# Kernel tuning notes

Hardware: AMD Instinct MI355X
Metric: run time of the kernel (lower is better)

Reference implementation:

```python
import jax, jax.numpy as jnp
import numpy as np

B, I, H, O, E, K = 1024, 512, 2048, 512, 8, 2


def setup_inputs() -> dict:
    key = jax.random.key(0)
    k = jax.random.split(key, 7)
    s = 0.02
    return {
        "x": jax.random.normal(k[0], (B, I), dtype=jnp.float32),
        "Wg": jax.random.normal(k[1], (I, E), dtype=jnp.float32) * s,
        "bg": jnp.zeros((E,), dtype=jnp.float32),
        "W1": jax.random.normal(k[2], (E, I, H), dtype=jnp.float32) * s,
        "b1": jnp.zeros((E, H), dtype=jnp.float32),
        "W2": jax.random.normal(k[3], (E, H, O), dtype=jnp.float32) * s,
        "b2": jnp.zeros((E, O), dtype=jnp.float32),
    }


def reference(x, Wg, bg, W1, b1, W2, b2):
    # Gating: linear -> softmax -> top-k -> renormalize (inference path,
    # no dynamic expert creation / sleep bookkeeping).
    logits = x @ Wg + bg                      # [B, E]
    probs = jax.nn.softmax(logits, axis=-1)
    top_w, top_i = jax.lax.top_k(probs, K)    # [B, K]
    top_w = top_w / jnp.sum(top_w, axis=-1, keepdims=True)
    # Dense combine weights: zero for unselected experts -> identical math to
    # the per-expert mask-gather / weighted scatter-add in the torch loop.
    combine = jnp.zeros((x.shape[0], W1.shape[0]), dtype=x.dtype)
    combine = combine.at[jnp.arange(x.shape[0])[:, None], top_i].add(top_w)  # [B, E]
    # Expert MLPs (Linear -> ReLU -> Linear), batched over experts.
    h = jax.nn.relu(jnp.einsum("bi,eih->beh", x, W1) + b1[None])  # [B, E, H]
    y = jnp.einsum("beh,eho->beo", h, W2) + b2[None]              # [B, E, O]
    out = jnp.einsum("be,beo->bo", combine, y)                    # [B, O]
    return out
```

## Files before the change

### kernel.cpp

```cpp
#include <hip/hip_runtime.h>
#include <math.h>


#define B_TOK 1024
#define I_DIM 512
#define H_DIM 2048
#define O_DIM 512
#define E_NUM 8
#define CAP   1024

#define WS_COUNTS   0
#define WS_TOK_E    64
#define WS_TOK_W    8256
#define WS_TOK_SLOT 16448
#define WS_XB       65536
#define WS_HB       (WS_XB + 1048576)
#define WS_Y2       (WS_HB + 33554432)

typedef __attribute__((ext_vector_type(8))) __bf16 bf16x8;
typedef __attribute__((ext_vector_type(4))) __bf16 bf16x4;
typedef __attribute__((ext_vector_type(2))) __bf16 bf16x2;
typedef __attribute__((ext_vector_type(4))) float f32x4;

#define MFMA16 __builtin_amdgcn_mfma_f32_16x16x32_bf16

__global__ __launch_bounds__(256) void gating_kernel(
    const float* __restrict__ x, const float* __restrict__ Wg,
    const float* __restrict__ bg, __bf16* __restrict__ xb,
    int* __restrict__ tok_e, float* __restrict__ tok_w)
{
    const int lane = threadIdx.x & 63;
    const int t = blockIdx.x * 4 + (threadIdx.x >> 6);
    const float4* x4 = (const float4*)(x + (size_t)t * I_DIM);
    float4 va = x4[lane], vb = x4[lane + 64];
    bf16x4 oa, ob;
    oa[0] = (__bf16)va.x; oa[1] = (__bf16)va.y;
    oa[2] = (__bf16)va.z; oa[3] = (__bf16)va.w;
    ob[0] = (__bf16)vb.x; ob[1] = (__bf16)vb.y;
    ob[2] = (__bf16)vb.z; ob[3] = (__bf16)vb.w;
    *(bf16x4*)(xb + (size_t)t * I_DIM + lane * 4) = oa;
    *(bf16x4*)(xb + (size_t)t * I_DIM + 256 + lane * 4) = ob;

    float acc[8];
#pragma unroll
    for (int e = 0; e < 8; ++e) acc[e] = 0.f;
    float xv[8] = {va.x, va.y, va.z, va.w, vb.x, vb.y, vb.z, vb.w};
#pragma unroll
    for (int u = 0; u < 8; ++u) {
        int i = (u < 4) ? (lane * 4 + u) : (256 + lane * 4 + u - 4);
        const float4* wr = (const float4*)(Wg + (size_t)i * 8);
        float4 wa = wr[0], wb2 = wr[1];
        acc[0] = fmaf(xv[u], wa.x, acc[0]);
        acc[1] = fmaf(xv[u], wa.y, acc[1]);
        acc[2] = fmaf(xv[u], wa.z, acc[2]);
        acc[3] = fmaf(xv[u], wa.w, acc[3]);
        acc[4] = fmaf(xv[u], wb2.x, acc[4]);
        acc[5] = fmaf(xv[u], wb2.y, acc[5]);
        acc[6] = fmaf(xv[u], wb2.z, acc[6]);
        acc[7] = fmaf(xv[u], wb2.w, acc[7]);
    }
#pragma unroll
    for (int off = 32; off > 0; off >>= 1)
#pragma unroll
        for (int e = 0; e < 8; ++e)
            acc[e] += __shfl_xor(acc[e], off, 64);
    if (lane == 0) {
        float l[8];
#pragma unroll
        for (int e = 0; e < 8; ++e) l[e] = acc[e] + bg[e];
        int e0 = 0;
        for (int e = 1; e < 8; ++e) if (l[e] > l[e0]) e0 = e;
        int e1 = (e0 == 0) ? 1 : 0;
        for (int e = 0; e < 8; ++e) {
            if (e == e0) continue;
            if (l[e] > l[e1]) e1 = e;
        }
        float w0 = 1.f / (1.f + expf(l[e1] - l[e0]));
        tok_e[t * 2]     = e0;
        tok_e[t * 2 + 1] = e1;
        tok_w[t * 2]     = w0;
        tok_w[t * 2 + 1] = 1.f - w0;
    }
}

template <bool IS_FC1>
__global__ __launch_bounds__(512) void moe_gemm(
    const __bf16* __restrict__ A, const float* __restrict__ Wf,
    const float* __restrict__ bias,
    int* __restrict__ counts, const int* __restrict__ tok_e,
    int* __restrict__ tok_slot,
    __bf16* __restrict__ hb, float* __restrict__ y2)
{
    constexpr int BN    = IS_FC1 ? 64 : 32;
    constexpr int KSPAN = IS_FC1 ? 512 : 1024;
    constexpr int BSTR  = KSPAN + 8;
    constexpr int NCH   = KSPAN / 256;
    constexpr int JN    = BN / 16;
    constexpr int C4N   = BN / 4;
    constexpr int NW    = IS_FC1 ? H_DIM : O_DIM;
    constexpr int ASTR  = IS_FC1 ? I_DIM : H_DIM;

    const int e  = blockIdx.z;
    const int kc = IS_FC1 ? 0 : (int)blockIdx.y;
    const int k0 = kc * KSPAN;
    const int n0 = blockIdx.x * BN;
    const int off = e * CAP;
    const float* W = Wf + (size_t)e * (IS_FC1 ? I_DIM * H_DIM : H_DIM * O_DIM);

    __shared__ __align__(16) __bf16 Bs[BN * BSTR];
    __shared__ int sl_tok[IS_FC1 ? CAP : 1];
    __shared__ int sMe;

    const int tid = threadIdx.x;
    const int lane = tid & 63, w = tid >> 6;
    const int l15 = lane & 15, q = lane >> 4;

    if (IS_FC1 && w == 0) {
        int cnt = 0;
#pragma unroll
        for (int b = 0; b < 2; ++b) {
            int vals[16];
#pragma unroll
            for (int c = 0; c < 16; ++c)
                vals[c] = tok_e[(b * 16 + c) * 64 + lane];
#pragma unroll
            for (int c = 0; c < 16; ++c) {
                const int gidx = (b * 16 + c) * 64 + lane;
                const bool hit = (vals[c] == e);
                const unsigned long long mk = __ballot(hit);
                if (hit) {
                    const int pos = cnt + __popcll(mk & ((1ull << lane) - 1));
                    sl_tok[pos] = gidx >> 1;
                    if (blockIdx.x == 0) tok_slot[gidx] = off + pos;
                }
                cnt += __popcll(mk);
            }
        }
        if (lane == 0) {
            sMe = cnt;
            if (blockIdx.x == 0) counts[e] = cnt;
        }
    }
    const int MeG = IS_FC1 ? 0 : counts[e];

    auto stage_chunk = [&](int ch) {
        const int kb = k0 + ch * 256;
#pragma unroll
        for (int i = 0; i < (128 * C4N) / 512; ++i) {
            const int u = tid + 512 * i;
            const int p = u / C4N, c4 = u % C4N;
            const float* wp = W + (size_t)(kb + 2 * p) * NW + n0 + c4 * 4;
            float4 r0 = *(const float4*)wp;
            float4 r1 = *(const float4*)(wp + NW);
            const float* f0 = (const float*)&r0;
            const float* f1 = (const float*)&r1;
#pragma unroll
            for (int j = 0; j < 4; ++j) {
                bf16x2 pk;
                pk[0] = (__bf16)f0[j];
                pk[1] = (__bf16)f1[j];
                *(bf16x2*)&Bs[(size_t)(c4 * 4 + j) * BSTR + ch * 256 + 2 * p] = pk;
            }
        }
    };

    stage_chunk(0);
    __syncthreads();
#pragma unroll
    for (int ch = 1; ch < NCH; ++ch) stage_chunk(ch);

    const int Me = IS_FC1 ? sMe : MeG;

    auto set_aptr = [&](int m0, const __bf16*& a0, const __bf16*& a1) {
        int mA = m0 + l15;      if (mA >= Me) mA = Me - 1;
        int mB = m0 + 16 + l15; if (mB >= Me) mB = Me - 1;
        if (IS_FC1) {
            a0 = A + (size_t)sl_tok[mA] * ASTR + q * 8;
            a1 = A + (size_t)sl_tok[mB] * ASTR + q * 8;
        } else {
            a0 = A + (size_t)(off + mA) * ASTR + k0 + q * 8;
            a1 = A + (size_t)(off + mB) * ASTR + k0 + q * 8;
        }
    };
    auto compute = [&](const __bf16* a0, const __bf16* a1,
                       f32x4 (&acc)[2][JN], int ks0, int ks1) {
#pragma unroll 4
        for (int ks = ks0; ks < ks1; ++ks) {
            bf16x8 af0 = *(const bf16x8*)(a0 + ks * 32);
            bf16x8 af1 = *(const bf16x8*)(a1 + ks * 32);
#pragma unroll
            for (int jj = 0; jj < JN; ++jj) {
                bf16x8 bf = *(const bf16x8*)
                    &Bs[(size_t)(jj * 16 + l15) * BSTR + ks * 32 + q * 8];
                acc[0][jj] = MFMA16(af0, bf, acc[0][jj], 0, 0, 0);
                acc[1][jj] = MFMA16(af1, bf, acc[1][jj], 0, 0, 0);
            }
        }
    };
    auto epilogue = [&](int m0, f32x4 (&acc)[2][JN]) {
#pragma unroll
        for (int jj = 0; jj < JN; ++jj) {
            const int gn = n0 + jj * 16 + l15;
            if (IS_FC1) {
                const float bv = bias[e * H_DIM + gn];
#pragma unroll
                for (int i = 0; i < 2; ++i)
#pragma unroll
                    for (int r = 0; r < 4; ++r) {
                        int m = m0 + i * 16 + q * 4 + r;
                        if (m < Me) {
                            float v = acc[i][jj][r] + bv;
                            hb[(size_t)(off + m) * H_DIM + gn] =
                                (__bf16)fmaxf(v, 0.f);
                        }
                    }
            } else {
#pragma unroll
                for (int i = 0; i < 2; ++i)
#pragma unroll
                    for (int r = 0; r < 4; ++r) {
                        int m = m0 + i * 16 + q * 4 + r;
                        if (m < Me)
                            y2[((size_t)kc * (E_NUM * CAP) + off + m) * O_DIM + gn] =
                                acc[i][jj][r];
                    }
            }
        }
    };

    const bool act0 = (w * 32 < Me);
    int m0 = w * 32;
    f32x4 acc[2][JN] = {};
    const __bf16 *a0 = nullptr, *a1 = nullptr;
    if (act0) {
        set_aptr(m0, a0, a1);
        compute(a0, a1, acc, 0, 8);
    }
    __syncthreads();
    if (act0) {
        compute(a0, a1, acc, 8, KSPAN / 32);
        epilogue(m0, acc);
    }
    for (m0 = w * 32 + 256; m0 < Me; m0 += 256) {
        f32x4 acc2[2][JN] = {};
        set_aptr(m0, a0, a1);
        compute(a0, a1, acc2, 0, KSPAN / 32);
        epilogue(m0, acc2);
    }
}

__global__ __launch_bounds__(256) void combine_kernel(
    const float* __restrict__ y2, const float* __restrict__ b2,
    const int* __restrict__ tok_slot, const int* __restrict__ tok_e,
    const float* __restrict__ tok_w, float* __restrict__ out)
{
    const int idx = blockIdx.x * 256 + threadIdx.x;
    const int t = idx >> 7;
    const int c = (idx & 127) * 4;
    float4 sum = {0.f, 0.f, 0.f, 0.f};
#pragma unroll
    for (int k = 0; k < 2; ++k) {
        const int s = tok_slot[t * 2 + k];
        const int e = tok_e[t * 2 + k];
        const float wgt = tok_w[t * 2 + k];
        float4 a = *(const float4*)(b2 + (size_t)e * O_DIM + c);
#pragma unroll
        for (int kc = 0; kc < 2; ++kc) {
            float4 v = *(const float4*)
                (y2 + ((size_t)kc * (E_NUM * CAP) + s) * O_DIM + c);
            a.x += v.x; a.y += v.y; a.z += v.z; a.w += v.w;
        }
        sum.x += wgt * a.x; sum.y += wgt * a.y;
        sum.z += wgt * a.z; sum.w += wgt * a.w;
    }
    *(float4*)(out + (size_t)t * O_DIM + c) = sum;
}

extern "C" void kernel_launch(void* const* d_in, const int* in_sizes, int n_in,
                              void* d_out, int out_size, void* d_ws, size_t ws_size,
                              hipStream_t stream)
{
    const float* x  = (const float*)d_in[0];
    const float* Wg = (const float*)d_in[1];
    const float* bg = (const float*)d_in[2];
    const float* W1 = (const float*)d_in[3];
    const float* b1 = (const float*)d_in[4];
    const float* W2 = (const float*)d_in[5];
    const float* b2 = (const float*)d_in[6];
    float* out = (float*)d_out;
    char* ws = (char*)d_ws;

    int*    counts   = (int*)(ws + WS_COUNTS);
    int*    tok_e    = (int*)(ws + WS_TOK_E);
    float*  tok_w    = (float*)(ws + WS_TOK_W);
    int*    tok_slot = (int*)(ws + WS_TOK_SLOT);
    __bf16* xb       = (__bf16*)(ws + WS_XB);
    __bf16* hb       = (__bf16*)(ws + WS_HB);
    float*  y2       = (float*)(ws + WS_Y2);

    gating_kernel<<<B_TOK / 4, 256, 0, stream>>>(x, Wg, bg, xb, tok_e, tok_w);
    moe_gemm<true><<<dim3(32, 1, 8), 512, 0, stream>>>(
        xb, W1, b1, counts, tok_e, tok_slot, hb, y2);
    moe_gemm<false><<<dim3(16, 2, 8), 512, 0, stream>>>(
        hb, W2, b2, counts, tok_e, tok_slot, hb, y2);
    combine_kernel<<<(B_TOK * O_DIM / 4) / 256, 256, 0, stream>>>(
        y2, b2, tok_slot, tok_e, tok_w, out);
}
```

Baseline: 155.7 us.

## Fuse MoE gating, FC1, FC2 and combine into one cooperative kernel

Replaces the four separate launches with a single cooperative kernel of 256 blocks that uses grid-wide syncs between the gating, FC1, FC2 and combine phases. During gating, half the warps pre-stage the first half of the W1 tile into shared memory so weight loading overlaps the routing work. The aim is to remove per-launch overhead and the idle gaps between kernels. In exchange it pays for three grid barriers and is limited to one block per CU. If the cooperative launch fails, the original multi-kernel path still runs.

```diff
diff --git a/kernel.cpp b/kernel.cpp
--- a/kernel.cpp
+++ b/kernel.cpp
@@ -1,5 +1,8 @@
 #include <hip/hip_runtime.h>
+#include <hip/hip_cooperative_groups.h>
 #include <math.h>
+
+namespace cg = cooperative_groups;
 
 
 #define B_TOK 1024
@@ -23,6 +26,339 @@
 typedef __attribute__((ext_vector_type(4))) float f32x4;
 
 #define MFMA16 __builtin_amdgcn_mfma_f32_16x16x32_bf16
+
+#define BSTR1 520
+#define BSTR2 1032
+#define SMEM_BS    (64 * BSTR1 * 2)
+#define SMEM_BYTES (SMEM_BS + CAP * 4 + 16)
+
+__global__ __launch_bounds__(512) void moe_fused(
+    const float* __restrict__ x, const float* __restrict__ Wg,
+    const float* __restrict__ bg, const float* __restrict__ W1f,
+    const float* __restrict__ b1, const float* __restrict__ W2f,
+    const float* __restrict__ b2, float* __restrict__ out,
+    char* __restrict__ ws)
+{
+    int*    counts   = (int*)(ws + WS_COUNTS);
+    int*    tok_e    = (int*)(ws + WS_TOK_E);
+    float*  tok_w    = (float*)(ws + WS_TOK_W);
+    int*    tok_slot = (int*)(ws + WS_TOK_SLOT);
+    __bf16* xb       = (__bf16*)(ws + WS_XB);
+    __bf16* hb       = (__bf16*)(ws + WS_HB);
+    float*  y2       = (float*)(ws + WS_Y2);
+
+    __shared__ __align__(16) char smem[SMEM_BYTES];
+    __bf16* Bs     = (__bf16*)smem;
+    int*    sl_tok = (int*)(smem + SMEM_BS);
+    int*    sMe    = (int*)(smem + SMEM_BS + CAP * 4);
+
+    cg::grid_group grid = cg::this_grid();
+    const int tid  = threadIdx.x;
+    const int lane = tid & 63;
+    const int w    = tid >> 6;
+    const int bid  = blockIdx.x;
+    const int l15  = lane & 15, q = lane >> 4;
+
+    const int e1  = bid >> 5, nx1 = bid & 31;
+    const int n01 = nx1 * 64;
+    const float* W1 = W1f + (size_t)e1 * (I_DIM * H_DIM);
+
+    if (w < 4) {
+        const int t = bid * 4 + w;
+        const float4* x4 = (const float4*)(x + (size_t)t * I_DIM);
+        float4 va = x4[lane], vb = x4[lane + 64];
+        bf16x4 oa, ob;
+        oa[0] = (__bf16)va.x; oa[1] = (__bf16)va.y;
+        oa[2] = (__bf16)va.z; oa[3] = (__bf16)va.w;
+        ob[0] = (__bf16)vb.x; ob[1] = (__bf16)vb.y;
+        ob[2] = (__bf16)vb.z; ob[3] = (__bf16)vb.w;
+        *(bf16x4*)(xb + (size_t)t * I_DIM + lane * 4) = oa;
+        *(bf16x4*)(xb + (size_t)t * I_DIM + 256 + lane * 4) = ob;
+
+        float gacc[8];
+#pragma unroll
+        for (int e = 0; e < 8; ++e) gacc[e] = 0.f;
+        float xv[8] = {va.x, va.y, va.z, va.w, vb.x, vb.y, vb.z, vb.w};
+#pragma unroll
+        for (int u = 0; u < 8; ++u) {
+            int i = (u < 4) ? (lane * 4 + u) : (256 + lane * 4 + u - 4);
+            const float4* wr = (const float4*)(Wg + (size_t)i * 8);
+            float4 wa = wr[0], wb2 = wr[1];
+            gacc[0] = fmaf(xv[u], wa.x, gacc[0]);
+            gacc[1] = fmaf(xv[u], wa.y, gacc[1]);
+            gacc[2] = fmaf(xv[u], wa.z, gacc[2]);
+            gacc[3] = fmaf(xv[u], wa.w, gacc[3]);
+            gacc[4] = fmaf(xv[u], wb2.x, gacc[4]);
+            gacc[5] = fmaf(xv[u], wb2.y, gacc[5]);
+            gacc[6] = fmaf(xv[u], wb2.z, gacc[6]);
+            gacc[7] = fmaf(xv[u], wb2.w, gacc[7]);
+        }
+#pragma unroll
+        for (int off = 32; off > 0; off >>= 1)
+#pragma unroll
+            for (int e = 0; e < 8; ++e)
+                gacc[e] += __shfl_xor(gacc[e], off, 64);
+        if (lane == 0) {
+            float l[8];
+#pragma unroll
+            for (int e = 0; e < 8; ++e) l[e] = gacc[e] + bg[e];
+            int E0 = 0;
+            for (int e = 1; e < 8; ++e) if (l[e] > l[E0]) E0 = e;
+            int E1 = (E0 == 0) ? 1 : 0;
+            for (int e = 0; e < 8; ++e) {
+                if (e == E0) continue;
+                if (l[e] > l[E1]) E1 = e;
+            }
+            float w0 = 1.f / (1.f + expf(l[E1] - l[E0]));
+            tok_e[t * 2]     = E0;
+            tok_e[t * 2 + 1] = E1;
+            tok_w[t * 2]     = w0;
+            tok_w[t * 2 + 1] = 1.f - w0;
+        }
+    } else {
+#pragma unroll
+        for (int i = 0; i < 8; ++i) {
+            const int u = (tid - 256) + 256 * i;
+            const int p = u >> 4, c4 = u & 15;
+            const float* wp = W1 + (size_t)(2 * p) * H_DIM + n01 + c4 * 4;
+            float4 r0 = *(const float4*)wp;
+            float4 r1 = *(const float4*)(wp + H_DIM);
+            const float* f0 = (const float*)&r0;
+            const float* f1 = (const float*)&r1;
+#pragma unroll
+            for (int j = 0; j < 4; ++j) {
+                bf16x2 pk;
+                pk[0] = (__bf16)f0[j];
+                pk[1] = (__bf16)f1[j];
+                *(bf16x2*)&Bs[(size_t)(c4 * 4 + j) * BSTR1 + 2 * p] = pk;
+            }
+        }
+    }
+    grid.sync();
+
+    {
+        if (w == 0) {
+            int cnt = 0;
+#pragma unroll
+            for (int b = 0; b < 2; ++b) {
+                int vals[16];
+#pragma unroll
+                for (int c = 0; c < 16; ++c)
+                    vals[c] = tok_e[(b * 16 + c) * 64 + lane];
+#pragma unroll
+                for (int c = 0; c < 16; ++c) {
+                    const int gidx = (b * 16 + c) * 64 + lane;
+                    const bool hit = (vals[c] == e1);
+                    const unsigned long long mk = __ballot(hit);
+                    if (hit) {
+                        const int pos = cnt + __popcll(mk & ((1ull << lane) - 1));
+                        sl_tok[pos] = gidx >> 1;
+                        if (nx1 == 0) tok_slot[gidx] = e1 * CAP + pos;
+                    }
+                    cnt += __popcll(mk);
+                }
+            }
+            if (lane == 0) {
+                sMe[0] = cnt;
+                if (nx1 == 0) counts[e1] = cnt;
+            }
+        }
+        __syncthreads();
+        const int Me  = sMe[0];
+        const int off = e1 * CAP;
+
+#pragma unroll
+        for (int i = 0; i < 4; ++i) {
+            const int u = tid + 512 * i;
+            const int p = u >> 4, c4 = u & 15;
+            const float* wp = W1 + (size_t)(256 + 2 * p) * H_DIM + n01 + c4 * 4;
+            float4 r0 = *(const float4*)wp;
+            float4 r1 = *(const float4*)(wp + H_DIM);
+            const float* f0 = (const float*)&r0;
+            const float* f1 = (const float*)&r1;
+#pragma unroll
+            for (int j = 0; j < 4; ++j) {
+                bf16x2 pk;
+                pk[0] = (__bf16)f0[j];
+                pk[1] = (__bf16)f1[j];
+                *(bf16x2*)&Bs[(size_t)(c4 * 4 + j) * BSTR1 + 256 + 2 * p] = pk;
+            }
+        }
+
+        auto aptrF = [&](int m0, const __bf16*& a0, const __bf16*& a1) {
+            int mA = m0 + l15;      if (mA >= Me) mA = Me - 1;
+            int mB = m0 + 16 + l15; if (mB >= Me) mB = Me - 1;
+            a0 = xb + (size_t)sl_tok[mA] * I_DIM + q * 8;
+            a1 = xb + (size_t)sl_tok[mB] * I_DIM + q * 8;
+        };
+        auto computeF = [&](const __bf16* a0, const __bf16* a1,
+                            f32x4 (&acc)[2][4], int ks0, int ks1) {
+#pragma unroll 4
+            for (int ks = ks0; ks < ks1; ++ks) {
+                bf16x8 af0 = *(const bf16x8*)(a0 + ks * 32);
+                bf16x8 af1 = *(const bf16x8*)(a1 + ks * 32);
+#pragma unroll
+                for (int jj = 0; jj < 4; ++jj) {
+                    bf16x8 bf = *(const bf16x8*)
+                        &Bs[(size_t)(jj * 16 + l15) * BSTR1 + ks * 32 + q * 8];
+                    acc[0][jj] = MFMA16(af0, bf, acc[0][jj], 0, 0, 0);
+                    acc[1][jj] = MFMA16(af1, bf, acc[1][jj], 0, 0, 0);
+                }
+            }
+        };
+        auto epiF = [&](int m0, f32x4 (&acc)[2][4]) {
+#pragma unroll
+            for (int jj = 0; jj < 4; ++jj) {
+                const int gn = n01 + jj * 16 + l15;
+                const float bv = b1[e1 * H_DIM + gn];
+#pragma unroll
+                for (int i2 = 0; i2 < 2; ++i2)
+#pragma unroll
+                    for (int r = 0; r < 4; ++r) {
+                        int m = m0 + i2 * 16 + q * 4 + r;
+                        if (m < Me) {
+                            float v = acc[i2][jj][r] + bv;
+                            hb[(size_t)(off + m) * H_DIM + gn] =
+                                (__bf16)fmaxf(v, 0.f);
+                        }
+                    }
+            }
+        };
+
+        const bool act0 = (w * 32 < Me);
+        f32x4 acc[2][4] = {};
+        const __bf16 *a0 = nullptr, *a1 = nullptr;
+        if (act0) {
+            aptrF(w * 32, a0, a1);
+            computeF(a0, a1, acc, 0, 8);
+        }
+        __syncthreads();
+        if (act0) {
+            computeF(a0, a1, acc, 8, 16);
+            epiF(w * 32, acc);
+        }
+        for (int m0 = w * 32 + 256; m0 < Me; m0 += 256) {
+            f32x4 acc2[2][4] = {};
+            aptrF(m0, a0, a1);
+            computeF(a0, a1, acc2, 0, 16);
+            epiF(m0, acc2);
+        }
+    }
+    grid.sync();
+
+    {
+        const int e  = bid >> 5, kc = (bid >> 4) & 1, nx = bid & 15;
+        const int Me = counts[e];
+        const int off = e * CAP;
+        const int k0 = kc * 1024;
+        const int n0 = nx * 32;
+        const float* W2 = W2f + (size_t)e * (H_DIM * O_DIM);
+
+        auto stage2 = [&](int ch) {
+            const int kb = k0 + ch * 256;
+#pragma unroll
+            for (int i = 0; i < 2; ++i) {
+                const int u = tid + 512 * i;
+                const int p = u >> 3, c4 = u & 7;
+                const float* wp = W2 + (size_t)(kb + 2 * p) * O_DIM + n0 + c4 * 4;
+                float4 r0 = *(const float4*)wp;
+                float4 r1 = *(const float4*)(wp + O_DIM);
+                const float* f0 = (const float*)&r0;
+                const float* f1 = (const float*)&r1;
+#pragma unroll
+                for (int j = 0; j < 4; ++j) {
+                    bf16x2 pk;
+                    pk[0] = (__bf16)f0[j];
+                    pk[1] = (__bf16)f1[j];
+                    *(bf16x2*)&Bs[(size_t)(c4 * 4 + j) * BSTR2 + ch * 256 + 2 * p] = pk;
+                }
+            }
+        };
+        stage2(0);
+        __syncthreads();
+        stage2(1); stage2(2); stage2(3);
+
+        auto aptr2 = [&](int m0, const __bf16*& a0, const __bf16*& a1) {
+            int mA = m0 + l15;      if (mA >= Me) mA = Me - 1;
+            int mB = m0 + 16 + l15; if (mB >= Me) mB = Me - 1;
+            a0 = hb + (size_t)(off + mA) * H_DIM + k0 + q * 8;
+            a1 = hb + (size_t)(off + mB) * H_DIM + k0 + q * 8;
+        };
+        auto compute2 = [&](const __bf16* a0, const __bf16* a1,
+                            f32x4 (&acc)[2][2], int ks0, int ks1) {
+#pragma unroll 4
+            for (int ks = ks0; ks < ks1; ++ks) {
+                bf16x8 af0 = *(const bf16x8*)(a0 + ks * 32);
+                bf16x8 af1 = *(const bf16x8*)(a1 + ks * 32);
+#pragma unroll
+                for (int jj = 0; jj < 2; ++jj) {
+                    bf16x8 bf = *(const bf16x8*)
+                        &Bs[(size_t)(jj * 16 + l15) * BSTR2 + ks * 32 + q * 8];
+                    acc[0][jj] = MFMA16(af0, bf, acc[0][jj], 0, 0, 0);
+                    acc[1][jj] = MFMA16(af1, bf, acc[1][jj], 0, 0, 0);
+                }
+            }
+        };
+        auto epi2 = [&](int m0, f32x4 (&acc)[2][2]) {
+#pragma unroll
+            for (int jj = 0; jj < 2; ++jj) {
+                const int gn = n0 + jj * 16 + l15;
+#pragma unroll
+                for (int i2 = 0; i2 < 2; ++i2)
+#pragma unroll
+                    for (int r = 0; r < 4; ++r) {
+                        int m = m0 + i2 * 16 + q * 4 + r;
+                        if (m < Me)
+                            y2[((size_t)kc * (E_NUM * CAP) + off + m) * O_DIM + gn] =
+                                acc[i2][jj][r];
+                    }
+            }
+        };
+
+        const bool act0 = (w * 32 < Me);
+        f32x4 acc[2][2] = {};
+        const __bf16 *a0 = nullptr, *a1 = nullptr;
+        if (act0) {
+            aptr2(w * 32, a0, a1);
+            compute2(a0, a1, acc, 0, 8);
+        }
+        __syncthreads();
+        if (act0) {
+            compute2(a0, a1, acc, 8, 32);
+            epi2(w * 32, acc);
+        }
+        for (int m0 = w * 32 + 256; m0 < Me; m0 += 256) {
+            f32x4 acc2[2][2] = {};
+            aptr2(m0, a0, a1);
+            compute2(a0, a1, acc2, 0, 32);
+            epi2(m0, acc2);
+        }
+    }
+    grid.sync();
+
+    {
+        const int idx = bid * 512 + tid;
+        const int t = idx >> 7;
+        const int c = (idx & 127) * 4;
+        float4 sum = {0.f, 0.f, 0.f, 0.f};
+#pragma unroll
+        for (int k = 0; k < 2; ++k) {
+            const int s = tok_slot[t * 2 + k];
+            const int e = tok_e[t * 2 + k];
+            const float wgt = tok_w[t * 2 + k];
+            float4 a = *(const float4*)(b2 + (size_t)e * O_DIM + c);
+#pragma unroll
+            for (int kc = 0; kc < 2; ++kc) {
+                float4 v = *(const float4*)
+                    (y2 + ((size_t)kc * (E_NUM * CAP) + s) * O_DIM + c);
+                a.x += v.x; a.y += v.y; a.z += v.z; a.w += v.w;
+            }
+            sum.x += wgt * a.x; sum.y += wgt * a.y;
+            sum.z += wgt * a.z; sum.w += wgt * a.w;
+        }
+        *(float4*)(out + (size_t)t * O_DIM + c) = sum;
+    }
+}
 
 __global__ __launch_bounds__(256) void gating_kernel(
     const float* __restrict__ x, const float* __restrict__ Wg,
@@ -40,7 +376,6 @@
     ob[2] = (__bf16)vb.z; ob[3] = (__bf16)vb.w;
     *(bf16x4*)(xb + (size_t)t * I_DIM + lane * 4) = oa;
     *(bf16x4*)(xb + (size_t)t * I_DIM + 256 + lane * 4) = ob;
-
     float acc[8];
 #pragma unroll
     for (int e = 0; e < 8; ++e) acc[e] = 0.f;
@@ -107,7 +442,7 @@
     const int off = e * CAP;
     const float* W = Wf + (size_t)e * (IS_FC1 ? I_DIM * H_DIM : H_DIM * O_DIM);
 
-    __shared__ __align__(16) __bf16 Bs[BN * BSTR];
+    __shared__ __align__(16) __bf16 Bsl[BN * BSTR];
     __shared__ int sl_tok[IS_FC1 ? CAP : 1];
     __shared__ int sMe;
 
@@ -159,7 +494,7 @@
                 bf16x2 pk;
                 pk[0] = (__bf16)f0[j];
                 pk[1] = (__bf16)f1[j];
-                *(bf16x2*)&Bs[(size_t)(c4 * 4 + j) * BSTR + ch * 256 + 2 * p] = pk;
+                *(bf16x2*)&Bsl[(size_t)(c4 * 4 + j) * BSTR + ch * 256 + 2 * p] = pk;
             }
         }
     };
@@ -191,7 +526,7 @@
 #pragma unroll
             for (int jj = 0; jj < JN; ++jj) {
                 bf16x8 bf = *(const bf16x8*)
-                    &Bs[(size_t)(jj * 16 + l15) * BSTR + ks * 32 + q * 8];
+                    &Bsl[(size_t)(jj * 16 + l15) * BSTR + ks * 32 + q * 8];
                 acc[0][jj] = MFMA16(af0, bf, acc[0][jj], 0, 0, 0);
                 acc[1][jj] = MFMA16(af1, bf, acc[1][jj], 0, 0, 0);
             }
@@ -290,6 +625,12 @@
     float* out = (float*)d_out;
     char* ws = (char*)d_ws;
 
+    void* args[] = {(void*)&x, (void*)&Wg, (void*)&bg, (void*)&W1, (void*)&b1,
+                    (void*)&W2, (void*)&b2, (void*)&out, (void*)&ws};
+    hipError_t err = hipLaunchCooperativeKernel(
+        (const void*)moe_fused, dim3(256), dim3(512), args, 0, stream);
+    if (err == hipSuccess) return;
+
     int*    counts   = (int*)(ws + WS_COUNTS);
     int*    tok_e    = (int*)(ws + WS_TOK_E);
     float*  tok_w    = (float*)(ws + WS_TOK_W);
```

Result: slower. 261.7 us (+68.1%).

## Pre-transpose expert weights to bf16 in a prep kernel and stream B from global

Applied to the files above, without the earlier changes.

Gating is merged into a new prep kernel that also converts W1 and W2 to bf16 and transposes them into workspace, using a padded shared-memory tile for the transpose. The FC1 and FC2 GEMMs no longer stage fp32 weights into LDS. They read the pre-transposed bf16 weights directly from global memory, and the grid is split over more M-blocks with 256-thread blocks. This moves the weight conversion out of the GEMMs and spreads work across more blocks, at the cost of an extra full pass writing weights to workspace and B-operand loads that now hit L2 instead of LDS.

```diff
diff --git a/kernel.cpp b/kernel.cpp
--- a/kernel.cpp
+++ b/kernel.cpp
@@ -14,8 +14,10 @@
 #define WS_TOK_W    8256
 #define WS_TOK_SLOT 16448
 #define WS_XB       65536
-#define WS_HB       (WS_XB + 1048576)
-#define WS_Y2       (WS_HB + 33554432)
+#define WS_W1T      1114112
+#define WS_W2T      17891328
+#define WS_HB       34668544
+#define WS_Y2       68222976
 
 typedef __attribute__((ext_vector_type(8))) __bf16 bf16x8;
 typedef __attribute__((ext_vector_type(4))) __bf16 bf16x4;
@@ -24,228 +26,246 @@
 
 #define MFMA16 __builtin_amdgcn_mfma_f32_16x16x32_bf16
 
-__global__ __launch_bounds__(256) void gating_kernel(
+__global__ __launch_bounds__(256) void prep_kernel(
     const float* __restrict__ x, const float* __restrict__ Wg,
-    const float* __restrict__ bg, __bf16* __restrict__ xb,
-    int* __restrict__ tok_e, float* __restrict__ tok_w)
-{
-    const int lane = threadIdx.x & 63;
-    const int t = blockIdx.x * 4 + (threadIdx.x >> 6);
-    const float4* x4 = (const float4*)(x + (size_t)t * I_DIM);
-    float4 va = x4[lane], vb = x4[lane + 64];
-    bf16x4 oa, ob;
-    oa[0] = (__bf16)va.x; oa[1] = (__bf16)va.y;
-    oa[2] = (__bf16)va.z; oa[3] = (__bf16)va.w;
-    ob[0] = (__bf16)vb.x; ob[1] = (__bf16)vb.y;
-    ob[2] = (__bf16)vb.z; ob[3] = (__bf16)vb.w;
-    *(bf16x4*)(xb + (size_t)t * I_DIM + lane * 4) = oa;
-    *(bf16x4*)(xb + (size_t)t * I_DIM + 256 + lane * 4) = ob;
-
-    float acc[8];
-#pragma unroll
-    for (int e = 0; e < 8; ++e) acc[e] = 0.f;
-    float xv[8] = {va.x, va.y, va.z, va.w, vb.x, vb.y, vb.z, vb.w};
-#pragma unroll
-    for (int u = 0; u < 8; ++u) {
-        int i = (u < 4) ? (lane * 4 + u) : (256 + lane * 4 + u - 4);
-        const float4* wr = (const float4*)(Wg + (size_t)i * 8);
-        float4 wa = wr[0], wb2 = wr[1];
-        acc[0] = fmaf(xv[u], wa.x, acc[0]);
-        acc[1] = fmaf(xv[u], wa.y, acc[1]);
-        acc[2] = fmaf(xv[u], wa.z, acc[2]);
-        acc[3] = fmaf(xv[u], wa.w, acc[3]);
-        acc[4] = fmaf(xv[u], wb2.x, acc[4]);
-        acc[5] = fmaf(xv[u], wb2.y, acc[5]);
-        acc[6] = fmaf(xv[u], wb2.z, acc[6]);
-        acc[7] = fmaf(xv[u], wb2.w, acc[7]);
-    }
-#pragma unroll
-    for (int off = 32; off > 0; off >>= 1)
-#pragma unroll
-        for (int e = 0; e < 8; ++e)
-            acc[e] += __shfl_xor(acc[e], off, 64);
-    if (lane == 0) {
-        float l[8];
-#pragma unroll
-        for (int e = 0; e < 8; ++e) l[e] = acc[e] + bg[e];
-        int e0 = 0;
-        for (int e = 1; e < 8; ++e) if (l[e] > l[e0]) e0 = e;
-        int e1 = (e0 == 0) ? 1 : 0;
-        for (int e = 0; e < 8; ++e) {
-            if (e == e0) continue;
-            if (l[e] > l[e1]) e1 = e;
-        }
-        float w0 = 1.f / (1.f + expf(l[e1] - l[e0]));
-        tok_e[t * 2]     = e0;
-        tok_e[t * 2 + 1] = e1;
-        tok_w[t * 2]     = w0;
-        tok_w[t * 2 + 1] = 1.f - w0;
-    }
-}
-
-template <bool IS_FC1>
-__global__ __launch_bounds__(512) void moe_gemm(
-    const __bf16* __restrict__ A, const float* __restrict__ Wf,
-    const float* __restrict__ bias,
-    int* __restrict__ counts, const int* __restrict__ tok_e,
-    int* __restrict__ tok_slot,
-    __bf16* __restrict__ hb, float* __restrict__ y2)
-{
-    constexpr int BN    = IS_FC1 ? 64 : 32;
-    constexpr int KSPAN = IS_FC1 ? 512 : 1024;
-    constexpr int BSTR  = KSPAN + 8;
-    constexpr int NCH   = KSPAN / 256;
-    constexpr int JN    = BN / 16;
-    constexpr int C4N   = BN / 4;
-    constexpr int NW    = IS_FC1 ? H_DIM : O_DIM;
-    constexpr int ASTR  = IS_FC1 ? I_DIM : H_DIM;
-
-    const int e  = blockIdx.z;
-    const int kc = IS_FC1 ? 0 : (int)blockIdx.y;
-    const int k0 = kc * KSPAN;
-    const int n0 = blockIdx.x * BN;
-    const int off = e * CAP;
-    const float* W = Wf + (size_t)e * (IS_FC1 ? I_DIM * H_DIM : H_DIM * O_DIM);
-
-    __shared__ __align__(16) __bf16 Bs[BN * BSTR];
-    __shared__ int sl_tok[IS_FC1 ? CAP : 1];
+    const float* __restrict__ bg, const float* __restrict__ W1f,
+    const float* __restrict__ W2f,
+    __bf16* __restrict__ xb, int* __restrict__ tok_e,
+    float* __restrict__ tok_w,
+    __bf16* __restrict__ W1T, __bf16* __restrict__ W2T)
+{
+    const int tid = threadIdx.x, lane = tid & 63, w = tid >> 6;
+    const int b = blockIdx.x;
+
+    if (b < 256) {
+        const int t = b * 4 + w;
+        const float4* x4 = (const float4*)(x + (size_t)t * I_DIM);
+        float4 va = x4[lane], vb = x4[lane + 64];
+        bf16x4 oa, ob;
+        oa[0] = (__bf16)va.x; oa[1] = (__bf16)va.y;
+        oa[2] = (__bf16)va.z; oa[3] = (__bf16)va.w;
+        ob[0] = (__bf16)vb.x; ob[1] = (__bf16)vb.y;
+        ob[2] = (__bf16)vb.z; ob[3] = (__bf16)vb.w;
+        *(bf16x4*)(xb + (size_t)t * I_DIM + lane * 4) = oa;
+        *(bf16x4*)(xb + (size_t)t * I_DIM + 256 + lane * 4) = ob;
+
+        float gacc[8];
+#pragma unroll
+        for (int e = 0; e < 8; ++e) gacc[e] = 0.f;
+        float xv[8] = {va.x, va.y, va.z, va.w, vb.x, vb.y, vb.z, vb.w};
+#pragma unroll
+        for (int u = 0; u < 8; ++u) {
+            int i = (u < 4) ? (lane * 4 + u) : (256 + lane * 4 + u - 4);
+            const float4* wr = (const float4*)(Wg + (size_t)i * 8);
+            float4 wa = wr[0], wb2 = wr[1];
+            gacc[0] = fmaf(xv[u], wa.x, gacc[0]);
+            gacc[1] = fmaf(xv[u], wa.y, gacc[1]);
+            gacc[2] = fmaf(xv[u], wa.z, gacc[2]);
+            gacc[3] = fmaf(xv[u], wa.w, gacc[3]);
+            gacc[4] = fmaf(xv[u], wb2.x, gacc[4]);
+            gacc[5] = fmaf(xv[u], wb2.y, gacc[5]);
+            gacc[6] = fmaf(xv[u], wb2.z, gacc[6]);
+            gacc[7] = fmaf(xv[u], wb2.w, gacc[7]);
+        }
+#pragma unroll
+        for (int off = 32; off > 0; off >>= 1)
+#pragma unroll
+            for (int e = 0; e < 8; ++e)
+                gacc[e] += __shfl_xor(gacc[e], off, 64);
+        if (lane == 0) {
+            float l[8];
+#pragma unroll
+            for (int e = 0; e < 8; ++e) l[e] = gacc[e] + bg[e];
+            int E0 = 0;
+            for (int e = 1; e < 8; ++e) if (l[e] > l[E0]) E0 = e;
+            int E1 = (E0 == 0) ? 1 : 0;
+            for (int e = 0; e < 8; ++e) {
+                if (e == E0) continue;
+                if (l[e] > l[E1]) E1 = e;
+            }
+            float w0 = 1.f / (1.f + expf(l[E1] - l[E0]));
+            tok_e[t * 2]     = E0;
+            tok_e[t * 2 + 1] = E1;
+            tok_w[t * 2]     = w0;
+            tok_w[t * 2 + 1] = 1.f - w0;
+        }
+    }
+
+    const float* src; __bf16* dst; int NWs, KT, k0, n0;
+    if (b < 512) {
+        const int e = b >> 6, t = b & 63;
+        src = W1f + (size_t)e * I_DIM * H_DIM;
+        dst = W1T + (size_t)e * H_DIM * I_DIM;
+        NWs = H_DIM; KT = I_DIM;
+        k0 = (t >> 3) * 64; n0 = (t & 7) * 256;
+    } else {
+        const int u = b - 512, e = u >> 6, t = u & 63;
+        src = W2f + (size_t)e * H_DIM * O_DIM;
+        dst = W2T + (size_t)e * O_DIM * H_DIM;
+        NWs = O_DIM; KT = H_DIM;
+        k0 = (t >> 1) * 64; n0 = (t & 1) * 256;
+    }
+    __shared__ uint32_t T[256 * 33];
+#pragma unroll
+    for (int i = 0; i < 8; ++i) {
+        const int u = tid + 256 * i;
+        const int p = u >> 6, c4 = u & 63;
+        const float* wp = src + (size_t)(k0 + 2 * p) * NWs + n0 + c4 * 4;
+        float4 r0 = *(const float4*)wp;
+        float4 r1 = *(const float4*)(wp + NWs);
+        const float* f0 = (const float*)&r0;
+        const float* f1 = (const float*)&r1;
+#pragma unroll
+        for (int j = 0; j < 4; ++j) {
+            bf16x2 pk;
+            pk[0] = (__bf16)f0[j];
+            pk[1] = (__bf16)f1[j];
+            *(bf16x2*)&T[(c4 * 4 + j) * 33 + p] = pk;
+        }
+    }
+    __syncthreads();
+#pragma unroll
+    for (int i = 0; i < 8; ++i) {
+        const int v = tid + 256 * i;
+        const int n = v >> 3, s = v & 7;
+        uint4 d;
+        d.x = T[n * 33 + s * 4 + 0];
+        d.y = T[n * 33 + s * 4 + 1];
+        d.z = T[n * 33 + s * 4 + 2];
+        d.w = T[n * 33 + s * 4 + 3];
+        *(uint4*)(dst + (size_t)(n0 + n) * KT + k0 + s * 8) = d;
+    }
+}
+
+__global__ __launch_bounds__(256) void fc1_kernel(
+    const __bf16* __restrict__ xb, const __bf16* __restrict__ W1T,
+    const float* __restrict__ b1, const int* __restrict__ tok_e,
+    int* __restrict__ counts, int* __restrict__ tok_slot,
+    __bf16* __restrict__ hb)
+{
+    const int tid = threadIdx.x, lane = tid & 63, w = tid >> 6;
+    const int l15 = lane & 15, q = lane >> 4;
+    const int e = blockIdx.z, my = blockIdx.y, nx = blockIdx.x;
+    const int n0 = nx * 64;
+
+    __shared__ int sl[CAP];
     __shared__ int sMe;
 
-    const int tid = threadIdx.x;
-    const int lane = tid & 63, w = tid >> 6;
-    const int l15 = lane & 15, q = lane >> 4;
-
-    if (IS_FC1 && w == 0) {
+    if (w == 0) {
         int cnt = 0;
 #pragma unroll
-        for (int b = 0; b < 2; ++b) {
+        for (int bb = 0; bb < 2; ++bb) {
             int vals[16];
 #pragma unroll
             for (int c = 0; c < 16; ++c)
-                vals[c] = tok_e[(b * 16 + c) * 64 + lane];
+                vals[c] = tok_e[(bb * 16 + c) * 64 + lane];
 #pragma unroll
             for (int c = 0; c < 16; ++c) {
-                const int gidx = (b * 16 + c) * 64 + lane;
+                const int gidx = (bb * 16 + c) * 64 + lane;
                 const bool hit = (vals[c] == e);
                 const unsigned long long mk = __ballot(hit);
                 if (hit) {
                     const int pos = cnt + __popcll(mk & ((1ull << lane) - 1));
-                    sl_tok[pos] = gidx >> 1;
-                    if (blockIdx.x == 0) tok_slot[gidx] = off + pos;
+                    sl[pos] = gidx >> 1;
+                    if (nx == 0 && my == 0) tok_slot[gidx] = e * CAP + pos;
                 }
                 cnt += __popcll(mk);
             }
         }
         if (lane == 0) {
             sMe = cnt;
-            if (blockIdx.x == 0) counts[e] = cnt;
-        }
-    }
-    const int MeG = IS_FC1 ? 0 : counts[e];
-
-    auto stage_chunk = [&](int ch) {
-        const int kb = k0 + ch * 256;
-#pragma unroll
-        for (int i = 0; i < (128 * C4N) / 512; ++i) {
-            const int u = tid + 512 * i;
-            const int p = u / C4N, c4 = u % C4N;
-            const float* wp = W + (size_t)(kb + 2 * p) * NW + n0 + c4 * 4;
-            float4 r0 = *(const float4*)wp;
-            float4 r1 = *(const float4*)(wp + NW);
-            const float* f0 = (const float*)&r0;
-            const float* f1 = (const float*)&r1;
-#pragma unroll
-            for (int j = 0; j < 4; ++j) {
-                bf16x2 pk;
-                pk[0] = (__bf16)f0[j];
-                pk[1] = (__bf16)f1[j];
-                *(bf16x2*)&Bs[(size_t)(c4 * 4 + j) * BSTR + ch * 256 + 2 * p] = pk;
-            }
-        }
-    };
-
-    stage_chunk(0);
+            if (nx == 0 && my == 0) counts[e] = cnt;
+        }
+    }
     __syncthreads();
-#pragma unroll
-    for (int ch = 1; ch < NCH; ++ch) stage_chunk(ch);
-
-    const int Me = IS_FC1 ? sMe : MeG;
-
-    auto set_aptr = [&](int m0, const __bf16*& a0, const __bf16*& a1) {
+    const int Me = sMe;
+
+    const __bf16* Wt  = W1T + (size_t)e * H_DIM * I_DIM;
+    const __bf16* bp0 = Wt + (size_t)(n0 + l15) * I_DIM + q * 8;
+
+    for (int m0 = my * 128 + w * 32; m0 < Me; m0 += 256) {
         int mA = m0 + l15;      if (mA >= Me) mA = Me - 1;
         int mB = m0 + 16 + l15; if (mB >= Me) mB = Me - 1;
-        if (IS_FC1) {
-            a0 = A + (size_t)sl_tok[mA] * ASTR + q * 8;
-            a1 = A + (size_t)sl_tok[mB] * ASTR + q * 8;
-        } else {
-            a0 = A + (size_t)(off + mA) * ASTR + k0 + q * 8;
-            a1 = A + (size_t)(off + mB) * ASTR + k0 + q * 8;
-        }
-    };
-    auto compute = [&](const __bf16* a0, const __bf16* a1,
-                       f32x4 (&acc)[2][JN], int ks0, int ks1) {
+        const __bf16* a0 = xb + (size_t)sl[mA] * I_DIM + q * 8;
+        const __bf16* a1 = xb + (size_t)sl[mB] * I_DIM + q * 8;
+        f32x4 acc[2][4] = {};
 #pragma unroll 4
-        for (int ks = ks0; ks < ks1; ++ks) {
+        for (int ks = 0; ks < 16; ++ks) {
             bf16x8 af0 = *(const bf16x8*)(a0 + ks * 32);
             bf16x8 af1 = *(const bf16x8*)(a1 + ks * 32);
 #pragma unroll
-            for (int jj = 0; jj < JN; ++jj) {
-                bf16x8 bf = *(const bf16x8*)
-                    &Bs[(size_t)(jj * 16 + l15) * BSTR + ks * 32 + q * 8];
+            for (int jj = 0; jj < 4; ++jj) {
+                bf16x8 bf = *(const bf16x8*)(bp0 + (size_t)jj * 16 * I_DIM + ks * 32);
                 acc[0][jj] = MFMA16(af0, bf, acc[0][jj], 0, 0, 0);
                 acc[1][jj] = MFMA16(af1, bf, acc[1][jj], 0, 0, 0);
             }
         }
-    };
-    auto epilogue = [&](int m0, f32x4 (&acc)[2][JN]) {
-#pragma unroll
-        for (int jj = 0; jj < JN; ++jj) {
+#pragma unroll
+        for (int jj = 0; jj < 4; ++jj) {
             const int gn = n0 + jj * 16 + l15;
-            if (IS_FC1) {
-                const float bv = bias[e * H_DIM + gn];
-#pragma unroll
-                for (int i = 0; i < 2; ++i)
-#pragma unroll
-                    for (int r = 0; r < 4; ++r) {
-                        int m = m0 + i * 16 + q * 4 + r;
-                        if (m < Me) {
-                            float v = acc[i][jj][r] + bv;
-                            hb[(size_t)(off + m) * H_DIM + gn] =
-                                (__bf16)fmaxf(v, 0.f);
-                        }
+            const float bv = b1[e * H_DIM + gn];
+#pragma unroll
+            for (int i = 0; i < 2; ++i)
+#pragma unroll
+                for (int r = 0; r < 4; ++r) {
+                    int m = m0 + i * 16 + q * 4 + r;
+                    if (m < Me) {
+                        float v = acc[i][jj][r] + bv;
+                        hb[(size_t)(e * CAP + m) * H_DIM + gn] =
+                            (__bf16)fmaxf(v, 0.f);
                     }
-            } else {
-#pragma unroll
-                for (int i = 0; i < 2; ++i)
-#pragma unroll
-                    for (int r = 0; r < 4; ++r) {
-                        int m = m0 + i * 16 + q * 4 + r;
-                        if (m < Me)
-                            y2[((size_t)kc * (E_NUM * CAP) + off + m) * O_DIM + gn] =
-                                acc[i][jj][r];
-                    }
+                }
+        }
+    }
+}
+
+__global__ __launch_bounds__(256) void fc2_kernel(
+    const __bf16* __restrict__ hb, const __bf16* __restrict__ W2T,
+    const int* __restrict__ counts, float* __restrict__ y2)
+{
+    const int tid = threadIdx.x, lane = tid & 63, w = tid >> 6;
+    const int l15 = lane & 15, q = lane >> 4;
+    const int e = blockIdx.z;
+    const int my = blockIdx.y & 1, kc = blockIdx.y >> 1;
+    const int n0 = blockIdx.x * 32;
+    const int k0 = kc * 1024;
+
+    const int Me = counts[e];
+    if (Me == 0) return;
+
+    const __bf16* Wt  = W2T + (size_t)e * O_DIM * H_DIM;
+    const __bf16* bp0 = Wt + (size_t)(n0 + l15) * H_DIM + k0 + q * 8;
+
+    for (int m0 = my * 128 + w * 32; m0 < Me; m0 += 256) {
+        int mA = m0 + l15;      if (mA >= Me) mA = Me - 1;
+        int mB = m0 + 16 + l15; if (mB >= Me) mB = Me - 1;
+        const __bf16* a0 = hb + (size_t)(e * CAP + mA) * H_DIM + k0 + q * 8;
+        const __bf16* a1 = hb + (size_t)(e * CAP + mB) * H_DIM + k0 + q * 8;
+        f32x4 acc[2][2] = {};
+#pragma unroll 4
+        for (int ks = 0; ks < 32; ++ks) {
+            bf16x8 af0 = *(const bf16x8*)(a0 + ks * 32);
+            bf16x8 af1 = *(const bf16x8*)(a1 + ks * 32);
+#pragma unroll
+            for (int jj = 0; jj < 2; ++jj) {
+                bf16x8 bf = *(const bf16x8*)(bp0 + (size_t)jj * 16 * H_DIM + ks * 32);
+                acc[0][jj] = MFMA16(af0, bf, acc[0][jj], 0, 0, 0);
+                acc[1][jj] = MFMA16(af1, bf, acc[1][jj], 0, 0, 0);
             }
         }
-    };
-
-    const bool act0 = (w * 32 < Me);
-    int m0 = w * 32;
-    f32x4 acc[2][JN] = {};
-    const __bf16 *a0 = nullptr, *a1 = nullptr;
-    if (act0) {
-        set_aptr(m0, a0, a1);
-        compute(a0, a1, acc, 0, 8);
-    }
-    __syncthreads();
-    if (act0) {
-        compute(a0, a1, acc, 8, KSPAN / 32);
-        epilogue(m0, acc);
-    }
-    for (m0 = w * 32 + 256; m0 < Me; m0 += 256) {
-        f32x4 acc2[2][JN] = {};
-        set_aptr(m0, a0, a1);
-        compute(a0, a1, acc2, 0, KSPAN / 32);
-        epilogue(m0, acc2);
+#pragma unroll
+        for (int jj = 0; jj < 2; ++jj) {
+            const int gn = n0 + jj * 16 + l15;
+#pragma unroll
+            for (int i = 0; i < 2; ++i)
+#pragma unroll
+                for (int r = 0; r < 4; ++r) {
+                    int m = m0 + i * 16 + q * 4 + r;
+                    if (m < Me)
+                        y2[((size_t)kc * (E_NUM * CAP) + e * CAP + m) * O_DIM + gn] =
+                            acc[i][jj][r];
+                }
+        }
     }
 }
 
@@ -295,14 +315,16 @@
     float*  tok_w    = (float*)(ws + WS_TOK_W);
     int*    tok_slot = (int*)(ws + WS_TOK_SLOT);
     __bf16* xb       = (__bf16*)(ws + WS_XB);
+    __bf16* W1T      = (__bf16*)(ws + WS_W1T);
+    __bf16* W2T      = (__bf16*)(ws + WS_W2T);
     __bf16* hb       = (__bf16*)(ws + WS_HB);
     float*  y2       = (float*)(ws + WS_Y2);
 
-    gating_kernel<<<B_TOK / 4, 256, 0, stream>>>(x, Wg, bg, xb, tok_e, tok_w);
-    moe_gemm<true><<<dim3(32, 1, 8), 512, 0, stream>>>(
-        xb, W1, b1, counts, tok_e, tok_slot, hb, y2);
-    moe_gemm<false><<<dim3(16, 2, 8), 512, 0, stream>>>(
-        hb, W2, b2, counts, tok_e, tok_slot, hb, y2);
+    prep_kernel<<<1024, 256, 0, stream>>>(x, Wg, bg, W1, W2,
+                                          xb, tok_e, tok_w, W1T, W2T);
+    fc1_kernel<<<dim3(32, 2, 8), 256, 0, stream>>>(
+        xb, W1T, b1, tok_e, counts, tok_slot, hb);
+    fc2_kernel<<<dim3(16, 4, 8), 256, 0, stream>>>(hb, W2T, counts, y2);
     combine_kernel<<<(B_TOK * O_DIM / 4) / 256, 256, 0, stream>>>(
         y2, b2, tok_slot, tok_e, tok_w, out);
 }
```

Result: slower. 195.9 us (+25.9%).

## Shrink MoE GEMM tiles to 32 columns, split FC2 K four ways, flatten grid

Applied to the files above, without the earlier changes.

Both expert GEMMs now use a uniform 32-column by 512-K tile, so FC1 launches 512 blocks instead of 256 and FC2 splits K into four chunks (512 blocks instead of 256). The grid is flattened with the expert index in the low bits, and the overlapped weight-staging/compute phase is removed in favour of one staging pass then compute. Launch bounds request higher occupancy. The intent is to fill more CUs and cut per-block weight staging. In exchange, FC1 redoes the token scan and A-row gathers in twice as many blocks, and the combine kernel reads four fp32 partial buffers instead of two.

```diff
diff --git a/kernel.cpp b/kernel.cpp
--- a/kernel.cpp
+++ b/kernel.cpp
@@ -14,8 +14,8 @@
 #define WS_TOK_W    8256
 #define WS_TOK_SLOT 16448
 #define WS_XB       65536
-#define WS_HB       (WS_XB + 1048576)
-#define WS_Y2       (WS_HB + 33554432)
+#define WS_HB       1114112
+#define WS_Y4       34668544
 
 typedef __attribute__((ext_vector_type(8))) __bf16 bf16x8;
 typedef __attribute__((ext_vector_type(4))) __bf16 bf16x4;
@@ -23,6 +23,7 @@
 typedef __attribute__((ext_vector_type(4))) float f32x4;
 
 #define MFMA16 __builtin_amdgcn_mfma_f32_16x16x32_bf16
+#define BSTR 520
 
 __global__ __launch_bounds__(256) void gating_kernel(
     const float* __restrict__ x, const float* __restrict__ Wg,
@@ -84,132 +85,118 @@
 }
 
 template <bool IS_FC1>
-__global__ __launch_bounds__(512) void moe_gemm(
+__global__ __launch_bounds__(512, 4) void moe_gemm(
     const __bf16* __restrict__ A, const float* __restrict__ Wf,
     const float* __restrict__ bias,
     int* __restrict__ counts, const int* __restrict__ tok_e,
     int* __restrict__ tok_slot,
-    __bf16* __restrict__ hb, float* __restrict__ y2)
-{
-    constexpr int BN    = IS_FC1 ? 64 : 32;
-    constexpr int KSPAN = IS_FC1 ? 512 : 1024;
-    constexpr int BSTR  = KSPAN + 8;
-    constexpr int NCH   = KSPAN / 256;
-    constexpr int JN    = BN / 16;
-    constexpr int C4N   = BN / 4;
-    constexpr int NW    = IS_FC1 ? H_DIM : O_DIM;
-    constexpr int ASTR  = IS_FC1 ? I_DIM : H_DIM;
-
-    const int e  = blockIdx.z;
-    const int kc = IS_FC1 ? 0 : (int)blockIdx.y;
-    const int k0 = kc * KSPAN;
-    const int n0 = blockIdx.x * BN;
+    __bf16* __restrict__ hb, float* __restrict__ y4)
+{
+    constexpr int NW   = IS_FC1 ? H_DIM : O_DIM;
+    constexpr int ASTR = IS_FC1 ? I_DIM : H_DIM;
+
+    const int bid = blockIdx.x;
+    const int e = bid & 7;
+    const int r = bid >> 3;
+    const int nx = IS_FC1 ? r : (r & 15);
+    const int kc = IS_FC1 ? 0 : (r >> 4);
+    const int n0 = nx * 32;
+    const int kb = kc * 512;
     const int off = e * CAP;
     const float* W = Wf + (size_t)e * (IS_FC1 ? I_DIM * H_DIM : H_DIM * O_DIM);
 
-    __shared__ __align__(16) __bf16 Bs[BN * BSTR];
-    __shared__ int sl_tok[IS_FC1 ? CAP : 1];
+    __shared__ __align__(16) __bf16 Bs[32 * BSTR];
+    __shared__ int sl[IS_FC1 ? CAP : 1];
     __shared__ int sMe;
 
     const int tid = threadIdx.x;
     const int lane = tid & 63, w = tid >> 6;
     const int l15 = lane & 15, q = lane >> 4;
 
+#pragma unroll
+    for (int i = 0; i < 4; ++i) {
+        const int u = tid + 512 * i;
+        const int p = u >> 3, c4 = u & 7;
+        const float* wp = W + (size_t)(kb + 2 * p) * NW + n0 + c4 * 4;
+        float4 r0 = *(const float4*)wp;
+        float4 r1 = *(const float4*)(wp + NW);
+        const float* f0 = (const float*)&r0;
+        const float* f1 = (const float*)&r1;
+#pragma unroll
+        for (int j = 0; j < 4; ++j) {
+            bf16x2 pk;
+            pk[0] = (__bf16)f0[j];
+            pk[1] = (__bf16)f1[j];
+            *(bf16x2*)&Bs[(size_t)(c4 * 4 + j) * BSTR + 2 * p] = pk;
+        }
+    }
+
     if (IS_FC1 && w == 0) {
         int cnt = 0;
 #pragma unroll
-        for (int b = 0; b < 2; ++b) {
+        for (int bb = 0; bb < 2; ++bb) {
             int vals[16];
 #pragma unroll
             for (int c = 0; c < 16; ++c)
-                vals[c] = tok_e[(b * 16 + c) * 64 + lane];
+                vals[c] = tok_e[(bb * 16 + c) * 64 + lane];
 #pragma unroll
             for (int c = 0; c < 16; ++c) {
-                const int gidx = (b * 16 + c) * 64 + lane;
+                const int gidx = (bb * 16 + c) * 64 + lane;
                 const bool hit = (vals[c] == e);
                 const unsigned long long mk = __ballot(hit);
                 if (hit) {
                     const int pos = cnt + __popcll(mk & ((1ull << lane) - 1));
-                    sl_tok[pos] = gidx >> 1;
-                    if (blockIdx.x == 0) tok_slot[gidx] = off + pos;
+                    sl[pos] = gidx >> 1;
+                    if (nx == 0) tok_slot[gidx] = off + pos;
                 }
                 cnt += __popcll(mk);
             }
         }
         if (lane == 0) {
             sMe = cnt;
-            if (blockIdx.x == 0) counts[e] = cnt;
-        }
-    }
-    const int MeG = IS_FC1 ? 0 : counts[e];
-
-    auto stage_chunk = [&](int ch) {
-        const int kb = k0 + ch * 256;
-#pragma unroll
-        for (int i = 0; i < (128 * C4N) / 512; ++i) {
-            const int u = tid + 512 * i;
-            const int p = u / C4N, c4 = u % C4N;
-            const float* wp = W + (size_t)(kb + 2 * p) * NW + n0 + c4 * 4;
-            float4 r0 = *(const float4*)wp;
-            float4 r1 = *(const float4*)(wp + NW);
-            const float* f0 = (const float*)&r0;
-            const float* f1 = (const float*)&r1;
-#pragma unroll
-            for (int j = 0; j < 4; ++j) {
-                bf16x2 pk;
-                pk[0] = (__bf16)f0[j];
-                pk[1] = (__bf16)f1[j];
-                *(bf16x2*)&Bs[(size_t)(c4 * 4 + j) * BSTR + ch * 256 + 2 * p] = pk;
-            }
-        }
-    };
-
-    stage_chunk(0);
+            if (nx == 0) counts[e] = cnt;
+        }
+    }
     __syncthreads();
-#pragma unroll
-    for (int ch = 1; ch < NCH; ++ch) stage_chunk(ch);
-
-    const int Me = IS_FC1 ? sMe : MeG;
-
-    auto set_aptr = [&](int m0, const __bf16*& a0, const __bf16*& a1) {
+    const int Me = IS_FC1 ? sMe : counts[e];
+
+    for (int m0 = w * 32; m0 < Me; m0 += 256) {
         int mA = m0 + l15;      if (mA >= Me) mA = Me - 1;
         int mB = m0 + 16 + l15; if (mB >= Me) mB = Me - 1;
+        const __bf16 *a0, *a1;
         if (IS_FC1) {
-            a0 = A + (size_t)sl_tok[mA] * ASTR + q * 8;
-            a1 = A + (size_t)sl_tok[mB] * ASTR + q * 8;
+            a0 = A + (size_t)sl[mA] * ASTR + q * 8;
+            a1 = A + (size_t)sl[mB] * ASTR + q * 8;
         } else {
-            a0 = A + (size_t)(off + mA) * ASTR + k0 + q * 8;
-            a1 = A + (size_t)(off + mB) * ASTR + k0 + q * 8;
-        }
-    };
-    auto compute = [&](const __bf16* a0, const __bf16* a1,
-                       f32x4 (&acc)[2][JN], int ks0, int ks1) {
+            a0 = A + (size_t)(off + mA) * ASTR + kb + q * 8;
+            a1 = A + (size_t)(off + mB) * ASTR + kb + q * 8;
+        }
+
+        f32x4 acc[2][2] = {};
 #pragma unroll 4
-        for (int ks = ks0; ks < ks1; ++ks) {
+        for (int ks = 0; ks < 16; ++ks) {
             bf16x8 af0 = *(const bf16x8*)(a0 + ks * 32);
             bf16x8 af1 = *(const bf16x8*)(a1 + ks * 32);
 #pragma unroll
-            for (int jj = 0; jj < JN; ++jj) {
+            for (int jj = 0; jj < 2; ++jj) {
                 bf16x8 bf = *(const bf16x8*)
                     &Bs[(size_t)(jj * 16 + l15) * BSTR + ks * 32 + q * 8];
                 acc[0][jj] = MFMA16(af0, bf, acc[0][jj], 0, 0, 0);
                 acc[1][jj] = MFMA16(af1, bf, acc[1][jj], 0, 0, 0);
             }
         }
-    };
-    auto epilogue = [&](int m0, f32x4 (&acc)[2][JN]) {
-#pragma unroll
-        for (int jj = 0; jj < JN; ++jj) {
+#pragma unroll
+        for (int jj = 0; jj < 2; ++jj) {
             const int gn = n0 + jj * 16 + l15;
             if (IS_FC1) {
                 const float bv = bias[e * H_DIM + gn];
 #pragma unroll
                 for (int i = 0; i < 2; ++i)
 #pragma unroll
-                    for (int r = 0; r < 4; ++r) {
-                        int m = m0 + i * 16 + q * 4 + r;
+                    for (int rr = 0; rr < 4; ++rr) {
+                        int m = m0 + i * 16 + q * 4 + rr;
                         if (m < Me) {
-                            float v = acc[i][jj][r] + bv;
+                            float v = acc[i][jj][rr] + bv;
                             hb[(size_t)(off + m) * H_DIM + gn] =
                                 (__bf16)fmaxf(v, 0.f);
                         }
@@ -218,39 +205,19 @@
 #pragma unroll
                 for (int i = 0; i < 2; ++i)
 #pragma unroll
-                    for (int r = 0; r < 4; ++r) {
-                        int m = m0 + i * 16 + q * 4 + r;
+                    for (int rr = 0; rr < 4; ++rr) {
+                        int m = m0 + i * 16 + q * 4 + rr;
                         if (m < Me)
-                            y2[((size_t)kc * (E_NUM * CAP) + off + m) * O_DIM + gn] =
-                                acc[i][jj][r];
+                            y4[((size_t)kc * (E_NUM * CAP) + off + m) * O_DIM + gn] =
+                                acc[i][jj][rr];
                     }
             }
         }
-    };
-
-    const bool act0 = (w * 32 < Me);
-    int m0 = w * 32;
-    f32x4 acc[2][JN] = {};
-    const __bf16 *a0 = nullptr, *a1 = nullptr;
-    if (act0) {
-        set_aptr(m0, a0, a1);
-        compute(a0, a1, acc, 0, 8);
-    }
-    __syncthreads();
-    if (act0) {
-        compute(a0, a1, acc, 8, KSPAN / 32);
-        epilogue(m0, acc);
-    }
-    for (m0 = w * 32 + 256; m0 < Me; m0 += 256) {
-        f32x4 acc2[2][JN] = {};
-        set_aptr(m0, a0, a1);
-        compute(a0, a1, acc2, 0, KSPAN / 32);
-        epilogue(m0, acc2);
     }
 }
 
 __global__ __launch_bounds__(256) void combine_kernel(
-    const float* __restrict__ y2, const float* __restrict__ b2,
+    const float* __restrict__ y4, const float* __restrict__ b2,
     const int* __restrict__ tok_slot, const int* __restrict__ tok_e,
     const float* __restrict__ tok_w, float* __restrict__ out)
 {
@@ -265,9 +232,9 @@
         const float wgt = tok_w[t * 2 + k];
         float4 a = *(const float4*)(b2 + (size_t)e * O_DIM + c);
 #pragma unroll
-        for (int kc = 0; kc < 2; ++kc) {
+        for (int kc = 0; kc < 4; ++kc) {
             float4 v = *(const float4*)
-                (y2 + ((size_t)kc * (E_NUM * CAP) + s) * O_DIM + c);
+                (y4 + ((size_t)kc * (E_NUM * CAP) + s) * O_DIM + c);
             a.x += v.x; a.y += v.y; a.z += v.z; a.w += v.w;
         }
         sum.x += wgt * a.x; sum.y += wgt * a.y;
@@ -296,13 +263,13 @@
     int*    tok_slot = (int*)(ws + WS_TOK_SLOT);
     __bf16* xb       = (__bf16*)(ws + WS_XB);
     __bf16* hb       = (__bf16*)(ws + WS_HB);
-    float*  y2       = (float*)(ws + WS_Y2);
+    float*  y4       = (float*)(ws + WS_Y4);
 
     gating_kernel<<<B_TOK / 4, 256, 0, stream>>>(x, Wg, bg, xb, tok_e, tok_w);
-    moe_gemm<true><<<dim3(32, 1, 8), 512, 0, stream>>>(
-        xb, W1, b1, counts, tok_e, tok_slot, hb, y2);
-    moe_gemm<false><<<dim3(16, 2, 8), 512, 0, stream>>>(
-        hb, W2, b2, counts, tok_e, tok_slot, hb, y2);
+    moe_gemm<true><<<512, 512, 0, stream>>>(
+        xb, W1, b1, counts, tok_e, tok_slot, hb, y4);
+    moe_gemm<false><<<512, 512, 0, stream>>>(
+        hb, W2, b2, counts, tok_e, tok_slot, hb, y4);
     combine_kernel<<<(B_TOK * O_DIM / 4) / 256, 256, 0, stream>>>(
-        y2, b2, tok_slot, tok_e, tok_w, out);
-}
+        y4, b2, tok_slot, tok_e, tok_w, out);
+}
```

New measurement: 154.9 us. Within noise of the previous version (-0.5%).
